# Performance work log

Measured on AMD Instinct MI355X. Metric: run time of the kernel, lower is better.

Reference implementation:

```python
import jax, jax.numpy as jnp
import numpy as np

NX = NY = NZ = 256   # linear_freqs
D1 = D2 = D3 = 8     # reduced_freqs
DF = 16              # feature_dim
NPTS = 131072


def softplus_b10(x):
    # torch F.softplus(x, beta=10, threshold=1)
    bx = 10.0 * x
    return jnp.where(bx > 1.0, x, 0.1 * jnp.log1p(jnp.exp(jnp.minimum(bx, 30.0))))


def grid_sample2d(vol, gx, gy):
    """Bilinear grid_sample, align_corners=True. vol:[C,H,W] (complex ok),
    gx,gy:[N] in [-1,1] (gx indexes W, gy indexes H). Returns [C,N]."""
    C, H, W = vol.shape
    ix = (gx + 1.0) * 0.5 * (W - 1)
    iy = (gy + 1.0) * 0.5 * (H - 1)
    x0f = jnp.floor(ix)
    y0f = jnp.floor(iy)
    wx = ix - x0f
    wy = iy - y0f
    x0 = jnp.clip(x0f.astype(jnp.int32), 0, W - 1)
    x1 = jnp.clip(x0 + 1, 0, W - 1)
    y0 = jnp.clip(y0f.astype(jnp.int32), 0, H - 1)
    y1 = jnp.clip(y0 + 1, 0, H - 1)
    v00 = vol[:, y0, x0]
    v01 = vol[:, y0, x1]
    v10 = vol[:, y1, x0]
    v11 = vol[:, y1, x1]
    return (v00 * (1 - wy) * (1 - wx) + v01 * (1 - wy) * wx
            + v10 * wy * (1 - wx) + v11 * wy * wx)


def batch_irfft(ph, x, ff, T):
    """ph:[D,d,N] complex, x:[N] in [-1,1], ff:[d] freqs. Returns [D,N]."""
    xx = (x + 1.0) * 0.5 * (T - 1) / T                    # [N]
    ang = 2.0 * np.pi * xx[:, None] * ff[None, :]         # [N,d]
    scale = jnp.where(ff > 0, 2.0, 1.0)
    tw_re = jnp.cos(ang) * scale
    tw_im = jnp.sin(ang) * scale
    return (jnp.einsum('dfn,nf->dn', ph.real, tw_re)
            - jnp.einsum('dfn,nf->dn', ph.imag, tw_im))


def setup_inputs() -> dict:
    key = jax.random.key(0)
    ks = jax.random.split(key, 8)
    inputs = jax.random.uniform(ks[0], (NPTS, 3), jnp.float32, minval=-1.0, maxval=1.0)
    s = 0.01
    Fx_re = jax.random.normal(ks[1], (1, DF, D1, NY, NZ), jnp.float32) * s
    Fx_im = jax.random.normal(ks[2], (1, DF, D1, NY, NZ), jnp.float32) * s
    Fy_re = jax.random.normal(ks[3], (1, DF, NX, D2, NZ), jnp.float32) * s
    Fy_im = jax.random.normal(ks[4], (1, DF, NX, D2, NZ), jnp.float32) * s
    Fz_re = jax.random.normal(ks[5], (1, DF, NX, NY, D3), jnp.float32) * s
    Fz_im = jax.random.normal(ks[6], (1, DF, NX, NY, D3), jnp.float32) * s
    alpha_params = jnp.array([0.001], jnp.float32)
    return {"inputs": inputs, "Fx_re": Fx_re, "Fx_im": Fx_im,
            "Fy_re": Fy_re, "Fy_im": Fy_im, "Fz_re": Fz_re, "Fz_im": Fz_im,
            "alpha_params": alpha_params}


def reference(inputs, Fx_re, Fx_im, Fy_re, Fy_im, Fz_re, Fz_im, alpha_params):
    alpha = softplus_b10(alpha_params)[0]
    Fx = (Fx_re + 1j * Fx_im) * alpha        # [1,D,d1,Ny,Nz]
    Fy = (Fy_re + 1j * Fy_im) * alpha        # [1,D,Nx,d2,Nz]
    Fz = (Fz_re + 1j * Fz_im) * alpha        # [1,D,Nx,Ny,d3]
    # inverse FFT over the two full (linear) spectral axes
    Fx = jnp.fft.ifftn(Fx, axes=(3, 4), norm='forward')
    Fy = jnp.fft.ifftn(Fy, axes=(2, 4), norm='forward')
    Fz = jnp.fft.ifftn(Fz, axes=(2, 3), norm='forward')
    xs, ys, zs = inputs[:, 0], inputs[:, 1], inputs[:, 2]
    N = inputs.shape[0]
    kx = jnp.arange(D1, dtype=jnp.float32)   # linear sampling axis [0,1,...]
    ky = jnp.arange(D2, dtype=jnp.float32)
    kz = jnp.arange(D3, dtype=jnp.float32)
    # complex bilinear gathers (H,W) = (Ny,Nz) / (Nx,Nz) / (Ny,Nx)
    fx = grid_sample2d(Fx.reshape(DF * D1, NY, NZ), zs, ys).reshape(DF, D1, N)
    fy = grid_sample2d(jnp.transpose(Fy, (0, 1, 3, 2, 4)).reshape(DF * D2, NX, NZ),
                       zs, xs).reshape(DF, D2, N)
    fz = grid_sample2d(jnp.transpose(Fz, (0, 1, 4, 3, 2)).reshape(DF * D3, NY, NX),
                       xs, ys).reshape(DF, D3, N)
    fxx = batch_irfft(fx, xs, kx, NX)
    fyy = batch_irfft(fy, ys, ky, NY)
    fzz = batch_irfft(fz, zs, kz, NZ)
    return (fxx + fyy + fzz).T               # [N, DF]
```

## Files before the change

kernel.cpp:

```cpp
#include <hip/hip_runtime.h>
#include <hip/hip_fp16.h>
#include <math.h>

#define NPTS 131072
#define RS 264

__device__ __forceinline__ float dev_alpha(const float* __restrict__ ap) {
    float x = ap[0];
    float bx = 10.0f * x;
    if (bx > 1.0f) return x;
    float e = expf(fminf(bx, 30.0f));
    return 0.1f * log1pf(e);
}

__device__ __forceinline__ __half2 bch(unsigned u) { return __builtin_bit_cast(__half2, u); }

__device__ __forceinline__ void fft16_reg(float* re, float* im) {
    #define SW(a,b) { float t=re[a]; re[a]=re[b]; re[b]=t; t=im[a]; im[a]=im[b]; im[b]=t; }
    SW(1,8) SW(2,4) SW(3,12) SW(5,10) SW(7,14) SW(11,13)
    #undef SW
    const float C[8] = {1.f, 0.9238795325112867f, 0.7071067811865476f, 0.3826834323650898f,
                        0.f, -0.3826834323650898f, -0.7071067811865476f, -0.9238795325112867f};
    const float S[8] = {0.f, 0.3826834323650898f, 0.7071067811865476f, 0.9238795325112867f,
                        1.f, 0.9238795325112867f, 0.7071067811865476f, 0.3826834323650898f};
    #pragma unroll
    for (int m = 1; m < 16; m <<= 1) {
        #pragma unroll
        for (int k = 0; k < 16; k += 2 * m) {
            #pragma unroll
            for (int j = 0; j < m; ++j) {
                float wc = C[j * (8 / m)], ws = S[j * (8 / m)];
                int i0 = k + j, i1 = i0 + m;
                float tr = re[i1] * wc - im[i1] * ws;
                float ti = re[i1] * ws + im[i1] * wc;
                re[i1] = re[i0] - tr; im[i1] = im[i0] - ti;
                re[i0] += tr;         im[i0] += ti;
            }
        }
    }
}

__device__ __forceinline__ void fft256_block8(float* lre, float* lim, int tid) {
    const int r = tid >> 4, s = tid & 15;
    float xr[16], xi[16];
    #pragma unroll
    for (int a = 0; a < 16; ++a) {
        xr[a] = lre[r * RS + 16 * a + s];
        xi[a] = lim[r * RS + 16 * a + s];
    }
    __syncthreads();
    fft16_reg(xr, xi);
    #pragma unroll
    for (int c = 0; c < 16; ++c) {
        float sn, cs;
        __sincosf(0.0245436926061703f * (float)(s * c), &sn, &cs);
        float tr = xr[c] * cs - xi[c] * sn;
        float ti = xr[c] * sn + xi[c] * cs;
        int idx = r * RS + 16 * c + (s ^ c);
        lre[idx] = tr; lim[idx] = ti;
    }
    __syncthreads();
    #pragma unroll
    for (int b = 0; b < 16; ++b) {
        int idx = r * RS + 16 * s + (b ^ s);
        xr[b] = lre[idx]; xi[b] = lim[idx];
    }
    __syncthreads();
    fft16_reg(xr, xi);
    __half2* hb = (__half2*)lre;
    #pragma unroll
    for (int d = 0; d < 16; ++d)
        hb[r * RS + 16 * d + s] = __floats2half2_rn(xr[d], xi[d]);
    __syncthreads();
}

__device__ __forceinline__ void dev_p1_xy(int bg, const float4* __restrict__ Fre4,
        const float4* __restrict__ Fim4, float alpha, uint4* __restrict__ GT4,
        int Sd4, int Sa4, float* lre, float* lim, int tid)
{
    const int d = bg & 7, ag = (bg >> 3) & 31, f = bg >> 8;
    const int a0 = ag * 8, c = f * 8 + d;
    const int base4 = f * 131072 + d * Sd4 + a0 * Sa4;
    #pragma unroll
    for (int j = 0; j < 4; ++j) {
        int i4 = tid + 128 * j;
        int ar = i4 >> 6, b4 = i4 & 63;
        float4 vr = Fre4[base4 + ar * Sa4 + b4];
        float4 vi = Fim4[base4 + ar * Sa4 + b4];
        int o = ar * RS + 4 * b4;
        *(float4*)&lre[o] = make_float4(vr.x*alpha, vr.y*alpha, vr.z*alpha, vr.w*alpha);
        *(float4*)&lim[o] = make_float4(vi.x*alpha, vi.y*alpha, vi.z*alpha, vi.w*alpha);
    }
    __syncthreads();
    fft256_block8(lre, lim, tid);
    const unsigned* hw = (const unsigned*)lre;
    const int g = tid >> 1, rq = tid & 1;
    #pragma unroll
    for (int j = 0; j < 4; ++j) {
        int k = g + 64 * j;
        uint4 ov = make_uint4(hw[(4*rq+0)*RS + k], hw[(4*rq+1)*RS + k],
                              hw[(4*rq+2)*RS + k], hw[(4*rq+3)*RS + k]);
        GT4[c * 16384 + k * 64 + ag * 2 + rq] = ov;
    }
}

__device__ __forceinline__ void dev_p2_xy(int bg, const uint4* __restrict__ GT4,
        uint4* __restrict__ V4, float* lre, float* lim, int tid)
{
    const int cg = bg & 15, b = bg >> 4, c0 = cg * 8;
    #pragma unroll
    for (int j = 0; j < 4; ++j) {
        int i4 = tid + 128 * j;
        int cr = i4 >> 6, a4 = i4 & 63;
        uint4 gv = GT4[(c0 + cr) * 16384 + b * 64 + a4];
        int o = cr * RS + 4 * a4;
        float2 e;
        e = __half22float2(bch(gv.x)); lre[o+0]=e.x; lim[o+0]=e.y;
        e = __half22float2(bch(gv.y)); lre[o+1]=e.x; lim[o+1]=e.y;
        e = __half22float2(bch(gv.z)); lre[o+2]=e.x; lim[o+2]=e.y;
        e = __half22float2(bch(gv.w)); lre[o+3]=e.x; lim[o+3]=e.y;
    }
    __syncthreads();
    fft256_block8(lre, lim, tid);
    const unsigned* hw = (const unsigned*)lre;
    const int g = tid >> 1, rq = tid & 1;
    #pragma unroll
    for (int j = 0; j < 4; ++j) {
        int k = g + 64 * j;
        uint4 ov = make_uint4(hw[(4*rq+0)*RS + k], hw[(4*rq+1)*RS + k],
                              hw[(4*rq+2)*RS + k], hw[(4*rq+3)*RS + k]);
        V4[(b * 256 + k) * 32 + cg * 2 + rq] = ov;
    }
}

__device__ __forceinline__ void dev_p1_z(int bg, const float4* __restrict__ Fre4,
        const float4* __restrict__ Fim4, float alpha, uint4* __restrict__ GTz4,
        float* lre, float* lim, int tid)
{
    const int f = bg >> 8, kx = bg & 255;
    const int base4 = f * 131072 + kx * 512;
    #pragma unroll
    for (int j = 0; j < 4; ++j) {
        int i4 = tid + 128 * j;
        int ky = i4 >> 1, t0 = i4 & 1;
        float4 vr = Fre4[base4 + i4];
        float4 vi = Fim4[base4 + i4];
        int r0 = 4 * t0;
        lre[(r0+0)*RS + ky] = vr.x*alpha; lim[(r0+0)*RS + ky] = vi.x*alpha;
        lre[(r0+1)*RS + ky] = vr.y*alpha; lim[(r0+1)*RS + ky] = vi.y*alpha;
        lre[(r0+2)*RS + ky] = vr.z*alpha; lim[(r0+2)*RS + ky] = vi.z*alpha;
        lre[(r0+3)*RS + ky] = vr.w*alpha; lim[(r0+3)*RS + ky] = vi.w*alpha;
    }
    __syncthreads();
    fft256_block8(lre, lim, tid);
    const unsigned* hw = (const unsigned*)lre;
    const int g = tid >> 1, rq = tid & 1;
    #pragma unroll
    for (int j = 0; j < 4; ++j) {
        int k = g + 64 * j;
        uint4 ov = make_uint4(hw[(4*rq+0)*RS + k], hw[(4*rq+1)*RS + k],
                              hw[(4*rq+2)*RS + k], hw[(4*rq+3)*RS + k]);
        GTz4[k * 8192 + f * 512 + kx * 2 + rq] = ov;
    }
}

__device__ __forceinline__ void dev_p2_z(int bg, const uint4* __restrict__ GTz4,
        uint4* __restrict__ V4, float* lre, float* lim, int tid)
{
    const int fg = bg & 15, b = bg >> 4;
    const int base4 = b * 8192 + fg * 512;
    #pragma unroll
    for (int j = 0; j < 4; ++j) {
        int i4 = tid + 128 * j;
        int kx = i4 >> 1, t0 = i4 & 1;
        uint4 gv = GTz4[base4 + i4];
        int r0 = 4 * t0;
        float2 e;
        e = __half22float2(bch(gv.x)); lre[(r0+0)*RS + kx]=e.x; lim[(r0+0)*RS + kx]=e.y;
        e = __half22float2(bch(gv.y)); lre[(r0+1)*RS + kx]=e.x; lim[(r0+1)*RS + kx]=e.y;
        e = __half22float2(bch(gv.z)); lre[(r0+2)*RS + kx]=e.x; lim[(r0+2)*RS + kx]=e.y;
        e = __half22float2(bch(gv.w)); lre[(r0+3)*RS + kx]=e.x; lim[(r0+3)*RS + kx]=e.y;
    }
    __syncthreads();
    fft256_block8(lre, lim, tid);
    const unsigned* hw = (const unsigned*)lre;
    const int g = tid >> 1, rq = tid & 1;
    #pragma unroll
    for (int j = 0; j < 4; ++j) {
        int k = g + 64 * j;
        uint4 ov = make_uint4(hw[(4*rq+0)*RS + k], hw[(4*rq+1)*RS + k],
                              hw[(4*rq+2)*RS + k], hw[(4*rq+3)*RS + k]);
        V4[(b * 256 + k) * 32 + fg * 2 + rq] = ov;
    }
}

__global__ __launch_bounds__(128) void fft_pass1_all(
    const float4* __restrict__ Fxr, const float4* __restrict__ Fxi,
    const float4* __restrict__ Fyr, const float4* __restrict__ Fyi,
    const float4* __restrict__ Fzr, const float4* __restrict__ Fzi,
    const float* __restrict__ alpha_p,
    uint4* __restrict__ GTx, uint4* __restrict__ GTy, uint4* __restrict__ GTz)
{
    __shared__ __align__(16) float lre[8 * RS];
    __shared__ __align__(16) float lim[8 * RS];
    const int tid = threadIdx.x, bg = blockIdx.x;
    const float alpha = dev_alpha(alpha_p);
    if (bg < 4096)       dev_p1_xy(bg,        Fxr, Fxi, alpha, GTx, 16384, 64,  lre, lim, tid);
    else if (bg < 8192)  dev_p1_xy(bg - 4096, Fyr, Fyi, alpha, GTy, 64,    512, lre, lim, tid);
    else                 dev_p1_z (bg - 8192, Fzr, Fzi, alpha, GTz,            lre, lim, tid);
}

__global__ __launch_bounds__(128) void fft_pass2_all(
    const uint4* __restrict__ GTx, const uint4* __restrict__ GTy, const uint4* __restrict__ GTz,
    uint4* __restrict__ Vx, uint4* __restrict__ Vy, uint4* __restrict__ Vz)
{
    __shared__ __align__(16) float lre[8 * RS];
    __shared__ __align__(16) float lim[8 * RS];
    const int tid = threadIdx.x, bg = blockIdx.x;
    if (bg < 4096)       dev_p2_xy(bg,        GTx, Vx, lre, lim, tid);
    else if (bg < 8192)  dev_p2_xy(bg - 4096, GTy, Vy, lre, lim, tid);
    else                 dev_p2_z (bg - 8192, GTz, Vz, lre, lim, tid);
}

__global__ __launch_bounds__(128) void fft_p1xy_k(
    const float4* __restrict__ Fre4, const float4* __restrict__ Fim4,
    const float* __restrict__ alpha_p, uint4* __restrict__ GT4, int Sd4, int Sa4)
{
    __shared__ __align__(16) float lre[8 * RS];
    __shared__ __align__(16) float lim[8 * RS];
    dev_p1_xy(blockIdx.x, Fre4, Fim4, dev_alpha(alpha_p), GT4, Sd4, Sa4, lre, lim, threadIdx.x);
}
__global__ __launch_bounds__(128) void fft_p2xy_k(
    const uint4* __restrict__ GT4, uint4* __restrict__ V4)
{
    __shared__ __align__(16) float lre[8 * RS];
    __shared__ __align__(16) float lim[8 * RS];
    dev_p2_xy(blockIdx.x, GT4, V4, lre, lim, threadIdx.x);
}
__global__ __launch_bounds__(128) void fft_p1z_k(
    const float4* __restrict__ Fre4, const float4* __restrict__ Fim4,
    const float* __restrict__ alpha_p, uint4* __restrict__ GTz4)
{
    __shared__ __align__(16) float lre[8 * RS];
    __shared__ __align__(16) float lim[8 * RS];
    dev_p1_z(blockIdx.x, Fre4, Fim4, dev_alpha(alpha_p), GTz4, lre, lim, threadIdx.x);
}
__global__ __launch_bounds__(128) void fft_p2z_k(
    const uint4* __restrict__ GTz4, uint4* __restrict__ V4)
{
    __shared__ __align__(16) float lre[8 * RS];
    __shared__ __align__(16) float lim[8 * RS];
    dev_p2_z(blockIdx.x, GTz4, V4, lre, lim, threadIdx.x);
}

__device__ __forceinline__ int bin8(float v) {
    return min(max((int)((v + 1.0f) * 127.5f), 0), 255);
}
__global__ __launch_bounds__(256) void zero_hist(unsigned* __restrict__ h) {
    h[blockIdx.x * 256 + threadIdx.x] = 0;
}
__global__ __launch_bounds__(256) void hist_k(const float* __restrict__ pts, unsigned* __restrict__ h) {
    int pid = blockIdx.x * 256 + threadIdx.x;
    int key = bin8(pts[pid * 3 + 2]) * 256 + bin8(pts[pid * 3 + 1]);
    atomicAdd(&h[key], 1u);
}
__global__ __launch_bounds__(256) void scan_k(const unsigned* __restrict__ h, unsigned* __restrict__ cur) {
    __shared__ unsigned part[256];
    const int t = threadIdx.x;
    unsigned sum = 0;
    for (int i = 0; i < 256; ++i) sum += h[t * 256 + i];
    part[t] = sum;
    __syncthreads();
    for (int o = 1; o < 256; o <<= 1) {
        unsigned v = part[t];
        unsigned add = (t >= o) ? part[t - o] : 0u;
        __syncthreads();
        part[t] = v + add;
        __syncthreads();
    }
    unsigned run = (t > 0) ? part[t - 1] : 0u;
    for (int i = 0; i < 256; ++i) {
        cur[t * 256 + i] = run;
        run += h[t * 256 + i];
    }
}
__global__ __launch_bounds__(256) void scatter_k(const float* __restrict__ pts,
                                                 unsigned* __restrict__ cur,
                                                 float4* __restrict__ ptsS) {
    int pid = blockIdx.x * 256 + threadIdx.x;
    float x = pts[pid * 3 + 0], y = pts[pid * 3 + 1], z = pts[pid * 3 + 2];
    int key = bin8(z) * 256 + bin8(y);
    unsigned pos = atomicAdd(&cur[key], 1u);
    ptsS[pos] = make_float4(x, y, z, __uint_as_float((unsigned)pid));
}

__device__ __forceinline__ void bsample4(const uint4* __restrict__ V,
        float gx, float gy, bool swap, int L, float* re, float* im)
{
    float ix = (gx + 1.0f) * 127.5f;
    float iy = (gy + 1.0f) * 127.5f;
    float x0f = floorf(ix), y0f = floorf(iy);
    float wx = ix - x0f, wy = iy - y0f;
    int x0 = min(max((int)x0f, 0), 255);
    int x1 = min(x0 + 1, 255);
    int y0 = min(max((int)y0f, 0), 255);
    int y1 = min(y0 + 1, 255);
    int rA, rB, rC, rD;
    if (swap) { rA = y0*256+x0; rB = y0*256+x1; rC = y1*256+x0; rD = y1*256+x1; }
    else      { rA = x0*256+y0; rB = x1*256+y0; rC = x0*256+y1; rD = x1*256+y1; }
    uint4 A = V[rA * 32 + L];
    uint4 B = V[rB * 32 + L];
    uint4 C = V[rC * 32 + L];
    uint4 D = V[rD * 32 + L];
    __half2 w00 = __float2half2_rn((1.0f - wy) * (1.0f - wx));
    __half2 w01 = __float2half2_rn((1.0f - wy) * wx);
    __half2 w10 = __float2half2_rn(wy * (1.0f - wx));
    __half2 w11 = __float2half2_rn(wy * wx);
    __half2 a0 = __hmul2(w00, bch(A.x)), a1 = __hmul2(w00, bch(A.y));
    __half2 a2 = __hmul2(w00, bch(A.z)), a3 = __hmul2(w00, bch(A.w));
    a0 = __hfma2(w01, bch(B.x), a0); a1 = __hfma2(w01, bch(B.y), a1);
    a2 = __hfma2(w01, bch(B.z), a2); a3 = __hfma2(w01, bch(B.w), a3);
    a0 = __hfma2(w10, bch(C.x), a0); a1 = __hfma2(w10, bch(C.y), a1);
    a2 = __hfma2(w10, bch(C.z), a2); a3 = __hfma2(w10, bch(C.w), a3);
    a0 = __hfma2(w11, bch(D.x), a0); a1 = __hfma2(w11, bch(D.y), a1);
    a2 = __hfma2(w11, bch(D.z), a2); a3 = __hfma2(w11, bch(D.w), a3);
    float2 e;
    e = __half22float2(a0); re[0] = e.x; im[0] = e.y;
    e = __half22float2(a1); re[1] = e.x; im[1] = e.y;
    e = __half22float2(a2); re[2] = e.x; im[2] = e.y;
    e = __half22float2(a3); re[3] = e.x; im[3] = e.y;
}

__device__ __forceinline__ float irdft4(const float* re, const float* im, float tw, int L)
{
    const float TWO_PI = 6.28318530717958647692f;
    float xx = (tw + 1.0f) * 0.5f * (255.0f / 256.0f);
    float th = TWO_PI * xx;
    int d0 = (L & 1) * 4;
    float s0, c0, st, ct;
    __sincosf(th * (float)d0, &s0, &c0);
    __sincosf(th, &st, &ct);
    float c = c0, s = s0;
    float p = 0.f;
    #pragma unroll
    for (int i = 0; i < 4; ++i) {
        p += 2.0f * (re[i] * c - im[i] * s);
        float cn = c * ct - s * st;
        s = s * ct + c * st;
        c = cn;
    }
    if (d0 == 0) p -= re[0];
    return p;
}

__global__ __launch_bounds__(256) void sample_all(
    const uint4* __restrict__ Vx, const uint4* __restrict__ Vy, const uint4* __restrict__ Vz,
    const float4* __restrict__ ptsS, float* __restrict__ out)
{
    const int lb = blockIdx.x;
    const int chunk = (lb & 7) * 2048 + (lb >> 3);
    const int tid = threadIdx.x;
    const int L = tid & 31;
    const int wid = chunk * 8 + (tid >> 5);
    float4 p = ptsS[wid];
    const float xs = p.x, ys = p.y, zs = p.z;
    const int pid = (int)__float_as_uint(p.w);

    float rex[4], imx[4], rey[4], imy[4], rez[4], imz[4];
    bsample4(Vx, zs, ys, false, L, rex, imx);
    bsample4(Vy, zs, xs, false, L, rey, imy);
    bsample4(Vz, xs, ys, true,  L, rez, imz);

    float pv = irdft4(rex, imx, xs, L) + irdft4(rey, imy, ys, L) + irdft4(rez, imz, zs, L);
    pv += __shfl_xor(pv, 1, 64);
    if ((L & 1) == 0) out[pid * 16 + (L >> 1)] = pv;
}

extern "C" void kernel_launch(void* const* d_in, const int* in_sizes, int n_in,
                              void* d_out, int out_size, void* d_ws, size_t ws_size,
                              hipStream_t stream) {
    const float* pts     = (const float*)d_in[0];
    const float4* Fxr    = (const float4*)d_in[1];
    const float4* Fxi    = (const float4*)d_in[2];
    const float4* Fyr    = (const float4*)d_in[3];
    const float4* Fyi    = (const float4*)d_in[4];
    const float4* Fzr    = (const float4*)d_in[5];
    const float4* Fzi    = (const float4*)d_in[6];
    const float* alpha_p = (const float*)d_in[7];
    float* out = (float*)d_out;

    char* ws = (char*)d_ws;
    const size_t MB = 1024 * 1024;
    uint4* Vx4 = (uint4*)(ws);
    uint4* Vy4 = (uint4*)(ws + 32 * MB);
    uint4* Vz4 = (uint4*)(ws + 64 * MB);

    size_t sortoff;
    if (ws_size >= (size_t)195 * MB) {
        uint4* GTx = (uint4*)(ws + 96 * MB);
        uint4* GTy = (uint4*)(ws + 128 * MB);
        uint4* GTz = (uint4*)(ws + 160 * MB);
        sortoff = 192 * MB;
        fft_pass1_all<<<12288, 128, 0, stream>>>(Fxr, Fxi, Fyr, Fyi, Fzr, Fzi, alpha_p,
                                                 GTx, GTy, GTz);
        fft_pass2_all<<<12288, 128, 0, stream>>>(GTx, GTy, GTz, Vx4, Vy4, Vz4);
    } else {
        uint4* GT = (uint4*)(ws + 96 * MB);
        sortoff = 96 * MB;
        fft_p1xy_k<<<4096, 128, 0, stream>>>(Fxr, Fxi, alpha_p, GT, 16384, 64);
        fft_p2xy_k<<<4096, 128, 0, stream>>>(GT, Vx4);
        fft_p1xy_k<<<4096, 128, 0, stream>>>(Fyr, Fyi, alpha_p, GT, 64, 512);
        fft_p2xy_k<<<4096, 128, 0, stream>>>(GT, Vy4);
        fft_p1z_k<<<4096, 128, 0, stream>>>(Fzr, Fzi, alpha_p, GT);
        fft_p2z_k<<<4096, 128, 0, stream>>>(GT, Vz4);
    }

    unsigned* hist = (unsigned*)(ws + sortoff);
    unsigned* cur  = (unsigned*)(ws + sortoff + 256 * 1024);
    float4*   ptsS = (float4*)  (ws + sortoff + 512 * 1024);
    zero_hist<<<256, 256, 0, stream>>>(hist);
    hist_k<<<NPTS / 256, 256, 0, stream>>>(pts, hist);
    scan_k<<<1, 256, 0, stream>>>(hist, cur);
    scatter_k<<<NPTS / 256, 256, 0, stream>>>(pts, cur, ptsS);

    sample_all<<<16384, 256, 0, stream>>>(Vx4, Vy4, Vz4, ptsS, out);
}
```

Measured before the change: 391.5 us.

## Rework 2D FFT passes to half2 LDS, 256-thread blocks and async global-to-LDS loads

Result: faster. 364.9 us (-6.8%).

```diff
diff --git a/kernel.cpp b/kernel.cpp
--- a/kernel.cpp
+++ b/kernel.cpp
@@ -3,7 +3,7 @@
 #include <math.h>
 
 #define NPTS 131072
-#define RS 264
+#define RSH 264
 
 __device__ __forceinline__ float dev_alpha(const float* __restrict__ ap) {
     float x = ap[0];
@@ -14,6 +14,13 @@
 }
 
 __device__ __forceinline__ __half2 bch(unsigned u) { return __builtin_bit_cast(__half2, u); }
+__device__ __forceinline__ unsigned packh2(float re, float im) {
+    return __builtin_bit_cast(unsigned, __floats2half2_rn(re, im));
+}
+__device__ __forceinline__ void gload_lds16(const uint4* __restrict__ g, unsigned* l) {
+    __builtin_amdgcn_global_load_lds((const __attribute__((address_space(1))) void*)g,
+                                     (__attribute__((address_space(3))) void*)l, 16, 0, 0);
+}
 
 __device__ __forceinline__ void fft16_reg(float* re, float* im) {
     #define SW(a,b) { float t=re[a]; re[a]=re[b]; re[b]=t; t=im[a]; im[a]=im[b]; im[b]=t; }
@@ -40,217 +47,171 @@
     }
 }
 
-__device__ __forceinline__ void fft256_block8(float* lre, float* lim, int tid) {
+__device__ __forceinline__ void fft256_h2(unsigned* lds, int tid, float scale) {
     const int r = tid >> 4, s = tid & 15;
+    unsigned* row = lds + r * RSH;
     float xr[16], xi[16];
     #pragma unroll
     for (int a = 0; a < 16; ++a) {
-        xr[a] = lre[r * RS + 16 * a + s];
-        xi[a] = lim[r * RS + 16 * a + s];
-    }
-    __syncthreads();
+        float2 e = __half22float2(bch(row[16 * a + s]));
+        xr[a] = e.x; xi[a] = e.y;
+    }
+    __builtin_amdgcn_wave_barrier();
     fft16_reg(xr, xi);
+    float ct, st;
+    __sincosf(0.0245436926061703f * (float)s, &st, &ct);
+    float cc = scale, sc = 0.f;
     #pragma unroll
     for (int c = 0; c < 16; ++c) {
-        float sn, cs;
-        __sincosf(0.0245436926061703f * (float)(s * c), &sn, &cs);
-        float tr = xr[c] * cs - xi[c] * sn;
-        float ti = xr[c] * sn + xi[c] * cs;
-        int idx = r * RS + 16 * c + (s ^ c);
-        lre[idx] = tr; lim[idx] = ti;
-    }
-    __syncthreads();
+        float tr = xr[c] * cc - xi[c] * sc;
+        float ti = xr[c] * sc + xi[c] * cc;
+        row[16 * c + (s ^ c)] = packh2(tr, ti);
+        float cn = cc * ct - sc * st;
+        sc = sc * ct + cc * st;
+        cc = cn;
+    }
+    __builtin_amdgcn_wave_barrier();
     #pragma unroll
     for (int b = 0; b < 16; ++b) {
-        int idx = r * RS + 16 * s + (b ^ s);
-        xr[b] = lre[idx]; xi[b] = lim[idx];
-    }
-    __syncthreads();
+        float2 e = __half22float2(bch(row[16 * s + (b ^ s)]));
+        xr[b] = e.x; xi[b] = e.y;
+    }
+    __builtin_amdgcn_wave_barrier();
     fft16_reg(xr, xi);
-    __half2* hb = (__half2*)lre;
     #pragma unroll
     for (int d = 0; d < 16; ++d)
-        hb[r * RS + 16 * d + s] = __floats2half2_rn(xr[d], xi[d]);
-    __syncthreads();
-}
-
-__device__ __forceinline__ void dev_p1_xy(int bg, const float4* __restrict__ Fre4,
+        row[16 * d + s] = packh2(xr[d], xi[d]);
+}
+
+__device__ __forceinline__ void writeout16(const unsigned* lds, int tid,
+                                           uint4* __restrict__ dst4,
+                                           int recStride4, int recOff4) {
+    const int g = tid >> 2, rq = tid & 3;
+    #pragma unroll
+    for (int j = 0; j < 4; ++j) {
+        int k = g + 64 * j;
+        uint4 ov = make_uint4(lds[(4 * rq + 0) * RSH + k], lds[(4 * rq + 1) * RSH + k],
+                              lds[(4 * rq + 2) * RSH + k], lds[(4 * rq + 3) * RSH + k]);
+        dst4[k * recStride4 + recOff4 + rq] = ov;
+    }
+}
+
+__device__ __forceinline__ void p1_xy(int bg, const float4* __restrict__ Fre4,
         const float4* __restrict__ Fim4, float alpha, uint4* __restrict__ GT4,
-        int Sd4, int Sa4, float* lre, float* lim, int tid)
-{
-    const int d = bg & 7, ag = (bg >> 3) & 31, f = bg >> 8;
-    const int a0 = ag * 8, c = f * 8 + d;
+        int Sd4, int Sa4, unsigned* lds, int tid)
+{
+    const int d = bg & 7, ag = (bg >> 3) & 15, f = bg >> 7;
+    const int a0 = ag * 16, c = f * 8 + d;
     const int base4 = f * 131072 + d * Sd4 + a0 * Sa4;
     #pragma unroll
     for (int j = 0; j < 4; ++j) {
-        int i4 = tid + 128 * j;
+        int i4 = tid + 256 * j;
         int ar = i4 >> 6, b4 = i4 & 63;
         float4 vr = Fre4[base4 + ar * Sa4 + b4];
         float4 vi = Fim4[base4 + ar * Sa4 + b4];
-        int o = ar * RS + 4 * b4;
-        *(float4*)&lre[o] = make_float4(vr.x*alpha, vr.y*alpha, vr.z*alpha, vr.w*alpha);
-        *(float4*)&lim[o] = make_float4(vi.x*alpha, vi.y*alpha, vi.z*alpha, vi.w*alpha);
-    }
-    __syncthreads();
-    fft256_block8(lre, lim, tid);
-    const unsigned* hw = (const unsigned*)lre;
-    const int g = tid >> 1, rq = tid & 1;
-    #pragma unroll
-    for (int j = 0; j < 4; ++j) {
-        int k = g + 64 * j;
-        uint4 ov = make_uint4(hw[(4*rq+0)*RS + k], hw[(4*rq+1)*RS + k],
-                              hw[(4*rq+2)*RS + k], hw[(4*rq+3)*RS + k]);
-        GT4[c * 16384 + k * 64 + ag * 2 + rq] = ov;
-    }
-}
-
-__device__ __forceinline__ void dev_p2_xy(int bg, const uint4* __restrict__ GT4,
-        uint4* __restrict__ V4, float* lre, float* lim, int tid)
-{
-    const int cg = bg & 15, b = bg >> 4, c0 = cg * 8;
-    #pragma unroll
-    for (int j = 0; j < 4; ++j) {
-        int i4 = tid + 128 * j;
-        int cr = i4 >> 6, a4 = i4 & 63;
-        uint4 gv = GT4[(c0 + cr) * 16384 + b * 64 + a4];
-        int o = cr * RS + 4 * a4;
-        float2 e;
-        e = __half22float2(bch(gv.x)); lre[o+0]=e.x; lim[o+0]=e.y;
-        e = __half22float2(bch(gv.y)); lre[o+1]=e.x; lim[o+1]=e.y;
-        e = __half22float2(bch(gv.z)); lre[o+2]=e.x; lim[o+2]=e.y;
-        e = __half22float2(bch(gv.w)); lre[o+3]=e.x; lim[o+3]=e.y;
-    }
-    __syncthreads();
-    fft256_block8(lre, lim, tid);
-    const unsigned* hw = (const unsigned*)lre;
-    const int g = tid >> 1, rq = tid & 1;
-    #pragma unroll
-    for (int j = 0; j < 4; ++j) {
-        int k = g + 64 * j;
-        uint4 ov = make_uint4(hw[(4*rq+0)*RS + k], hw[(4*rq+1)*RS + k],
-                              hw[(4*rq+2)*RS + k], hw[(4*rq+3)*RS + k]);
-        V4[(b * 256 + k) * 32 + cg * 2 + rq] = ov;
-    }
-}
-
-__device__ __forceinline__ void dev_p1_z(int bg, const float4* __restrict__ Fre4,
+        uint4 pk = make_uint4(packh2(vr.x, vi.x), packh2(vr.y, vi.y),
+                              packh2(vr.z, vi.z), packh2(vr.w, vi.w));
+        *(uint4*)&lds[ar * RSH + 4 * b4] = pk;
+    }
+    __syncthreads();
+    fft256_h2(lds, tid, alpha);
+    __syncthreads();
+    writeout16(lds, tid, GT4 + c * 16384, 64, ag * 4);
+}
+
+__device__ __forceinline__ void p2_xy(int bg, const uint4* __restrict__ GT4,
+        uint4* __restrict__ V4, unsigned* lds, int tid)
+{
+    const int cg = bg & 7, b = bg >> 3, c0 = cg * 16;
+    const int wv = __builtin_amdgcn_readfirstlane(tid >> 6);
+    const int lane = tid & 63;
+    #pragma unroll
+    for (int j = 0; j < 4; ++j) {
+        int cr = wv * 4 + j;
+        gload_lds16(GT4 + (c0 + cr) * 16384 + b * 64 + lane, &lds[cr * RSH]);
+    }
+    __syncthreads();
+    fft256_h2(lds, tid, 1.0f);
+    __syncthreads();
+    writeout16(lds, tid, V4 + b * 8192, 32, cg * 4);
+}
+
+__device__ __forceinline__ void p1_z(int bg, const float4* __restrict__ Fre4,
         const float4* __restrict__ Fim4, float alpha, uint4* __restrict__ GTz4,
-        float* lre, float* lim, int tid)
-{
-    const int f = bg >> 8, kx = bg & 255;
-    const int base4 = f * 131072 + kx * 512;
-    #pragma unroll
-    for (int j = 0; j < 4; ++j) {
-        int i4 = tid + 128 * j;
-        int ky = i4 >> 1, t0 = i4 & 1;
+        unsigned* lds, int tid)
+{
+    const int kxp = bg & 127, f = bg >> 7;
+    const int base4 = f * 131072 + kxp * 1024;
+    #pragma unroll
+    for (int j = 0; j < 4; ++j) {
+        int i4 = tid + 256 * j;
+        int kxo = i4 >> 9, rem = i4 & 511;
+        int ky = rem >> 1, t0 = rem & 1;
         float4 vr = Fre4[base4 + i4];
         float4 vi = Fim4[base4 + i4];
-        int r0 = 4 * t0;
-        lre[(r0+0)*RS + ky] = vr.x*alpha; lim[(r0+0)*RS + ky] = vi.x*alpha;
-        lre[(r0+1)*RS + ky] = vr.y*alpha; lim[(r0+1)*RS + ky] = vi.y*alpha;
-        lre[(r0+2)*RS + ky] = vr.z*alpha; lim[(r0+2)*RS + ky] = vi.z*alpha;
-        lre[(r0+3)*RS + ky] = vr.w*alpha; lim[(r0+3)*RS + ky] = vi.w*alpha;
-    }
-    __syncthreads();
-    fft256_block8(lre, lim, tid);
-    const unsigned* hw = (const unsigned*)lre;
-    const int g = tid >> 1, rq = tid & 1;
-    #pragma unroll
-    for (int j = 0; j < 4; ++j) {
-        int k = g + 64 * j;
-        uint4 ov = make_uint4(hw[(4*rq+0)*RS + k], hw[(4*rq+1)*RS + k],
-                              hw[(4*rq+2)*RS + k], hw[(4*rq+3)*RS + k]);
-        GTz4[k * 8192 + f * 512 + kx * 2 + rq] = ov;
-    }
-}
-
-__device__ __forceinline__ void dev_p2_z(int bg, const uint4* __restrict__ GTz4,
-        uint4* __restrict__ V4, float* lre, float* lim, int tid)
-{
-    const int fg = bg & 15, b = bg >> 4;
-    const int base4 = b * 8192 + fg * 512;
-    #pragma unroll
-    for (int j = 0; j < 4; ++j) {
-        int i4 = tid + 128 * j;
-        int kx = i4 >> 1, t0 = i4 & 1;
+        int r0 = kxo * 8 + 4 * t0;
+        lds[(r0 + 0) * RSH + ky] = packh2(vr.x, vi.x);
+        lds[(r0 + 1) * RSH + ky] = packh2(vr.y, vi.y);
+        lds[(r0 + 2) * RSH + ky] = packh2(vr.z, vi.z);
+        lds[(r0 + 3) * RSH + ky] = packh2(vr.w, vi.w);
+    }
+    __syncthreads();
+    fft256_h2(lds, tid, alpha);
+    __syncthreads();
+    writeout16(lds, tid, GTz4 + f * 512, 8192, kxp * 4);
+}
+
+__device__ __forceinline__ void p2_z(int bg, const uint4* __restrict__ GTz4,
+        uint4* __restrict__ V4, unsigned* lds, int tid)
+{
+    const int fg = bg & 7, b = bg >> 3;
+    const int base4 = b * 8192 + fg * 1024;
+    #pragma unroll
+    for (int j = 0; j < 4; ++j) {
+        int i4 = tid + 256 * j;
+        int fo = i4 >> 9, rem = i4 & 511;
+        int kx = rem >> 1, t0 = rem & 1;
         uint4 gv = GTz4[base4 + i4];
-        int r0 = 4 * t0;
-        float2 e;
-        e = __half22float2(bch(gv.x)); lre[(r0+0)*RS + kx]=e.x; lim[(r0+0)*RS + kx]=e.y;
-        e = __half22float2(bch(gv.y)); lre[(r0+1)*RS + kx]=e.x; lim[(r0+1)*RS + kx]=e.y;
-        e = __half22float2(bch(gv.z)); lre[(r0+2)*RS + kx]=e.x; lim[(r0+2)*RS + kx]=e.y;
-        e = __half22float2(bch(gv.w)); lre[(r0+3)*RS + kx]=e.x; lim[(r0+3)*RS + kx]=e.y;
-    }
-    __syncthreads();
-    fft256_block8(lre, lim, tid);
-    const unsigned* hw = (const unsigned*)lre;
-    const int g = tid >> 1, rq = tid & 1;
-    #pragma unroll
-    for (int j = 0; j < 4; ++j) {
-        int k = g + 64 * j;
-        uint4 ov = make_uint4(hw[(4*rq+0)*RS + k], hw[(4*rq+1)*RS + k],
-                              hw[(4*rq+2)*RS + k], hw[(4*rq+3)*RS + k]);
-        V4[(b * 256 + k) * 32 + fg * 2 + rq] = ov;
-    }
-}
-
-__global__ __launch_bounds__(128) void fft_pass1_all(
+        int r0 = fo * 8 + 4 * t0;
+        lds[(r0 + 0) * RSH + kx] = gv.x;
+        lds[(r0 + 1) * RSH + kx] = gv.y;
+        lds[(r0 + 2) * RSH + kx] = gv.z;
+        lds[(r0 + 3) * RSH + kx] = gv.w;
+    }
+    __syncthreads();
+    fft256_h2(lds, tid, 1.0f);
+    __syncthreads();
+    writeout16(lds, tid, V4 + b * 8192, 32, fg * 4);
+}
+
+__global__ __launch_bounds__(256, 4) void fft_pass1_all(
     const float4* __restrict__ Fxr, const float4* __restrict__ Fxi,
     const float4* __restrict__ Fyr, const float4* __restrict__ Fyi,
     const float4* __restrict__ Fzr, const float4* __restrict__ Fzi,
     const float* __restrict__ alpha_p,
-    uint4* __restrict__ GTx, uint4* __restrict__ GTy, uint4* __restrict__ GTz)
-{
-    __shared__ __align__(16) float lre[8 * RS];
-    __shared__ __align__(16) float lim[8 * RS];
-    const int tid = threadIdx.x, bg = blockIdx.x;
+    uint4* __restrict__ GTx, uint4* __restrict__ GTy, uint4* __restrict__ GTz,
+    int bgBase)
+{
+    __shared__ __align__(16) unsigned lds[16 * RSH];
+    const int tid = threadIdx.x;
+    const int bg = blockIdx.x + bgBase;
     const float alpha = dev_alpha(alpha_p);
-    if (bg < 4096)       dev_p1_xy(bg,        Fxr, Fxi, alpha, GTx, 16384, 64,  lre, lim, tid);
-    else if (bg < 8192)  dev_p1_xy(bg - 4096, Fyr, Fyi, alpha, GTy, 64,    512, lre, lim, tid);
-    else                 dev_p1_z (bg - 8192, Fzr, Fzi, alpha, GTz,            lre, lim, tid);
-}
-
-__global__ __launch_bounds__(128) void fft_pass2_all(
+    if (bg < 2048)       p1_xy(bg,        Fxr, Fxi, alpha, GTx, 16384, 64,  lds, tid);
+    else if (bg < 4096)  p1_xy(bg - 2048, Fyr, Fyi, alpha, GTy, 64,    512, lds, tid);
+    else                 p1_z (bg - 4096, Fzr, Fzi, alpha, GTz,            lds, tid);
+}
+
+__global__ __launch_bounds__(256, 4) void fft_pass2_all(
     const uint4* __restrict__ GTx, const uint4* __restrict__ GTy, const uint4* __restrict__ GTz,
-    uint4* __restrict__ Vx, uint4* __restrict__ Vy, uint4* __restrict__ Vz)
-{
-    __shared__ __align__(16) float lre[8 * RS];
-    __shared__ __align__(16) float lim[8 * RS];
-    const int tid = threadIdx.x, bg = blockIdx.x;
-    if (bg < 4096)       dev_p2_xy(bg,        GTx, Vx, lre, lim, tid);
-    else if (bg < 8192)  dev_p2_xy(bg - 4096, GTy, Vy, lre, lim, tid);
-    else                 dev_p2_z (bg - 8192, GTz, Vz, lre, lim, tid);
-}
-
-__global__ __launch_bounds__(128) void fft_p1xy_k(
-    const float4* __restrict__ Fre4, const float4* __restrict__ Fim4,
-    const float* __restrict__ alpha_p, uint4* __restrict__ GT4, int Sd4, int Sa4)
-{
-    __shared__ __align__(16) float lre[8 * RS];
-    __shared__ __align__(16) float lim[8 * RS];
-    dev_p1_xy(blockIdx.x, Fre4, Fim4, dev_alpha(alpha_p), GT4, Sd4, Sa4, lre, lim, threadIdx.x);
-}
-__global__ __launch_bounds__(128) void fft_p2xy_k(
-    const uint4* __restrict__ GT4, uint4* __restrict__ V4)
-{
-    __shared__ __align__(16) float lre[8 * RS];
-    __shared__ __align__(16) float lim[8 * RS];
-    dev_p2_xy(blockIdx.x, GT4, V4, lre, lim, threadIdx.x);
-}
-__global__ __launch_bounds__(128) void fft_p1z_k(
-    const float4* __restrict__ Fre4, const float4* __restrict__ Fim4,
-    const float* __restrict__ alpha_p, uint4* __restrict__ GTz4)
-{
-    __shared__ __align__(16) float lre[8 * RS];
-    __shared__ __align__(16) float lim[8 * RS];
-    dev_p1_z(blockIdx.x, Fre4, Fim4, dev_alpha(alpha_p), GTz4, lre, lim, threadIdx.x);
-}
-__global__ __launch_bounds__(128) void fft_p2z_k(
-    const uint4* __restrict__ GTz4, uint4* __restrict__ V4)
-{
-    __shared__ __align__(16) float lre[8 * RS];
-    __shared__ __align__(16) float lim[8 * RS];
-    dev_p2_z(blockIdx.x, GTz4, V4, lre, lim, threadIdx.x);
+    uint4* __restrict__ Vx, uint4* __restrict__ Vy, uint4* __restrict__ Vz,
+    int bgBase)
+{
+    __shared__ __align__(16) unsigned lds[16 * RSH];
+    const int tid = threadIdx.x;
+    const int bg = blockIdx.x + bgBase;
+    if (bg < 2048)       p2_xy(bg,        GTx, Vx, lds, tid);
+    else if (bg < 4096)  p2_xy(bg - 2048, GTy, Vy, lds, tid);
+    else                 p2_z (bg - 4096, GTz, Vz, lds, tid);
 }
 
 __device__ __forceinline__ int bin8(float v) {
@@ -401,18 +362,17 @@
         uint4* GTy = (uint4*)(ws + 128 * MB);
         uint4* GTz = (uint4*)(ws + 160 * MB);
         sortoff = 192 * MB;
-        fft_pass1_all<<<12288, 128, 0, stream>>>(Fxr, Fxi, Fyr, Fyi, Fzr, Fzi, alpha_p,
-                                                 GTx, GTy, GTz);
-        fft_pass2_all<<<12288, 128, 0, stream>>>(GTx, GTy, GTz, Vx4, Vy4, Vz4);
+        fft_pass1_all<<<6144, 256, 0, stream>>>(Fxr, Fxi, Fyr, Fyi, Fzr, Fzi, alpha_p,
+                                                GTx, GTy, GTz, 0);
+        fft_pass2_all<<<6144, 256, 0, stream>>>(GTx, GTy, GTz, Vx4, Vy4, Vz4, 0);
     } else {
         uint4* GT = (uint4*)(ws + 96 * MB);
         sortoff = 96 * MB;
-        fft_p1xy_k<<<4096, 128, 0, stream>>>(Fxr, Fxi, alpha_p, GT, 16384, 64);
-        fft_p2xy_k<<<4096, 128, 0, stream>>>(GT, Vx4);
-        fft_p1xy_k<<<4096, 128, 0, stream>>>(Fyr, Fyi, alpha_p, GT, 64, 512);
-        fft_p2xy_k<<<4096, 128, 0, stream>>>(GT, Vy4);
-        fft_p1z_k<<<4096, 128, 0, stream>>>(Fzr, Fzi, alpha_p, GT);
-        fft_p2z_k<<<4096, 128, 0, stream>>>(GT, Vz4);
+        for (int dir = 0; dir < 3; ++dir) {
+            fft_pass1_all<<<2048, 256, 0, stream>>>(Fxr, Fxi, Fyr, Fyi, Fzr, Fzi, alpha_p,
+                                                    GT, GT, GT, dir * 2048);
+            fft_pass2_all<<<2048, 256, 0, stream>>>(GT, GT, GT, Vx4, Vy4, Vz4, dir * 2048);
+        }
     }
 
     unsigned* hist = (unsigned*)(ws + sortoff);
```
